# Kernel optimization log

Hardware: AMD Instinct MI355X
Metric: run time of the kernel (lower is better)

## Reference

```python
import jax, jax.numpy as jnp
import numpy as np

B, S, D = 8, 2048, 256
H, HD = 4, 64  # num_heads, head_size; H*HD == D


def setup_inputs() -> dict:
    key = jax.random.key(0)
    ks = jax.random.split(key, 9)
    scale = 0.02
    return {
        "x": jax.random.normal(ks[0], (B, S, D), dtype=jnp.float32),
        "Wq": jax.random.normal(ks[1], (D, H * HD), dtype=jnp.float32) * scale,
        "bq": jnp.zeros((H * HD,), dtype=jnp.float32),
        "Wk": jax.random.normal(ks[2], (D, H * HD), dtype=jnp.float32) * scale,
        "bk": jnp.zeros((H * HD,), dtype=jnp.float32),
        "Wv": jax.random.normal(ks[3], (D, H * HD), dtype=jnp.float32) * scale,
        "bv": jnp.zeros((H * HD,), dtype=jnp.float32),
        "Wo": jax.random.normal(ks[4], (H * HD, D), dtype=jnp.float32) * scale,
        "bo": jnp.zeros((D,), dtype=jnp.float32),
    }


def _split_heads(t):
    # [B, S, H*HD] -> [B, H, S, HD]
    b, s, _ = t.shape
    return t.reshape(b, s, H, HD).transpose(0, 2, 1, 3)


def reference(x, Wq, bq, Wk, bk, Wv, bv, Wo, bo):
    q = _split_heads(x @ Wq + bq)
    k = _split_heads(x @ Wk + bk)
    v = _split_heads(x @ Wv + bv)
    scores = jnp.einsum("bhqd,bhkd->bhqk", q, k) / jnp.sqrt(jnp.float32(HD))
    weights = jax.nn.softmax(scores, axis=-1)
    attn = jnp.einsum("bhqk,bhkd->bhqd", weights, v)  # [B, H, S, HD]
    concat = attn.transpose(0, 2, 1, 3).reshape(x.shape[0], -1, H * HD)
    return concat @ Wo + bo
```

## Files before the change

kernel.cpp:

```cpp
#include <hip/hip_runtime.h>
#include <hip/hip_bf16.h>

namespace {

constexpr int B_ = 8, S = 2048, D = 256, H = 4, HD = 64;
constexpr int M = B_ * S;

typedef __attribute__((ext_vector_type(8))) short bf16x8;
typedef __attribute__((ext_vector_type(4))) short bf16x4;
typedef __attribute__((ext_vector_type(2))) short bf16x2;
typedef __attribute__((ext_vector_type(4))) float f32x4;
typedef __attribute__((ext_vector_type(16))) float f32x16;
typedef __attribute__((ext_vector_type(4))) unsigned uint4v;

__device__ inline short f2bf(float x) {
  __hip_bfloat16 h = __float2bfloat16(x);
  short s;
  __builtin_memcpy(&s, &h, 2);
  return s;
}

__device__ inline f32x4 mfma16(bf16x8 a, bf16x8 b, f32x4 c) {
  return __builtin_amdgcn_mfma_f32_16x16x32_bf16(a, b, c, 0, 0, 0);
}
__device__ inline f32x16 mfma32(bf16x8 a, bf16x8 b, f32x16 c) {
  return __builtin_amdgcn_mfma_f32_32x32x16_bf16(a, b, c, 0, 0, 0);
}

__device__ inline float exp2a(float x) {
  float r;
  asm("v_exp_f32 %0, %1" : "=v"(r) : "v"(x));
  return r;
}

__device__ inline unsigned pkbf(float lo, float hi) {
  bf16x2 t;
  t[0] = f2bf(lo);
  t[1] = f2bf(hi);
  unsigned u;
  __builtin_memcpy(&u, &t, 4);
  return u;
}

__global__ __launch_bounds__(256) void prep_kernel(
    const float* __restrict__ x,
    const float* __restrict__ Wq, const float* __restrict__ Wk,
    const float* __restrict__ Wv, const float* __restrict__ Wo,
    short* __restrict__ xbf,
    short* __restrict__ WqT, short* __restrict__ WkT,
    short* __restrict__ WvT, short* __restrict__ WoT) {
  const int blk = blockIdx.x, t = threadIdx.x;
  if (blk < 64) {
    const int wq = blk >> 4, n0 = (blk & 15) * 16;
    const float* W = wq == 0 ? Wq : wq == 1 ? Wk : wq == 2 ? Wv : Wo;
    short* Wt = wq == 0 ? WqT : wq == 1 ? WkT : wq == 2 ? WvT : WoT;
#pragma unroll
    for (int j4 = 0; j4 < 4; ++j4) {
      float4 v = *(const float4*)(W + (size_t)t * 256 + n0 + j4 * 4);
      Wt[(n0 + j4 * 4 + 0) * 256 + t] = f2bf(v.x);
      Wt[(n0 + j4 * 4 + 1) * 256 + t] = f2bf(v.y);
      Wt[(n0 + j4 * 4 + 2) * 256 + t] = f2bf(v.z);
      Wt[(n0 + j4 * 4 + 3) * 256 + t] = f2bf(v.w);
    }
  } else {
    size_t base = ((size_t)(blk - 64) * 256 + t) * 8;
    float4 a = *(const float4*)(x + base);
    float4 b = *(const float4*)(x + base + 4);
    bf16x8 r;
    r[0] = f2bf(a.x); r[1] = f2bf(a.y); r[2] = f2bf(a.z); r[3] = f2bf(a.w);
    r[4] = f2bf(b.x); r[5] = f2bf(b.y); r[6] = f2bf(b.z); r[7] = f2bf(b.w);
    *(bf16x8*)(xbf + base) = r;
  }
}

__global__ __launch_bounds__(256) void gemm_qkv_kernel(
    const short* __restrict__ xbf,
    const short* __restrict__ WqT, const short* __restrict__ WkT,
    const short* __restrict__ WvT,
    const float* __restrict__ bq, const float* __restrict__ bk,
    const float* __restrict__ bv,
    short* __restrict__ Qo, short* __restrict__ Ko, short* __restrict__ Vt) {
  const int bx = blockIdx.x;
  const int which = blockIdx.y;
  const short* Wt = which == 0 ? WqT : which == 1 ? WkT : WvT;
  const float* bias = which == 0 ? bq : which == 1 ? bk : bv;

  __shared__ short Xs[2][64 * 32];
  __shared__ short Ws[2][256 * 32];

  const int tid = threadIdx.x;
  const int wid = tid >> 6, lane = tid & 63;
  const int l15 = lane & 15, l4 = lane >> 4;
  const int nt0 = wid * 4;

  const short* xsrc = xbf + ((size_t)(bx * 64 + (tid >> 2))) * 256 + (tid & 3) * 8;
  const short* wsrc = Wt + ((size_t)(tid >> 2)) * 256 + (tid & 3) * 8;
  short* xdst0 = &Xs[0][tid * 8];
  short* xdst1 = &Xs[1][tid * 8];
  short* wdst0 = &Ws[0][tid * 8];
  short* wdst1 = &Ws[1][tid * 8];

  bf16x8 xr, wr[4];
  xr = *(const bf16x8*)xsrc;
#pragma unroll
  for (int p = 0; p < 4; ++p) wr[p] = *(const bf16x8*)(wsrc + (size_t)p * 64 * 256);
  *(bf16x8*)xdst0 = xr;
#pragma unroll
  for (int p = 0; p < 4; ++p) *(bf16x8*)(wdst0 + p * 2048) = wr[p];
  __syncthreads();

  f32x4 acc[4][4];
#pragma unroll
  for (int i = 0; i < 4; ++i)
#pragma unroll
    for (int mh = 0; mh < 4; ++mh) acc[i][mh] = f32x4{0.f, 0.f, 0.f, 0.f};

  for (int ks = 0; ks < 8; ++ks) {
    const int cur = ks & 1;
    if (ks < 7) {
      xr = *(const bf16x8*)(xsrc + (ks + 1) * 32);
#pragma unroll
      for (int p = 0; p < 4; ++p)
        wr[p] = *(const bf16x8*)(wsrc + (size_t)p * 64 * 256 + (ks + 1) * 32);
    }
    bf16x8 wf[4], xf[4];
#pragma unroll
    for (int i = 0; i < 4; ++i)
      wf[i] = *(const bf16x8*)&Ws[cur][((nt0 + i) * 16 + l15) * 32 + l4 * 8];
#pragma unroll
    for (int mh = 0; mh < 4; ++mh)
      xf[mh] = *(const bf16x8*)&Xs[cur][(mh * 16 + l15) * 32 + l4 * 8];
    if (which == 2) {
#pragma unroll
      for (int i = 0; i < 4; ++i)
#pragma unroll
        for (int mh = 0; mh < 4; ++mh)
          acc[i][mh] = mfma16(xf[mh], wf[i], acc[i][mh]);
    } else {
#pragma unroll
      for (int i = 0; i < 4; ++i)
#pragma unroll
        for (int mh = 0; mh < 4; ++mh)
          acc[i][mh] = mfma16(wf[i], xf[mh], acc[i][mh]);
    }
    if (ks < 7) {
      short* xd = (cur ? xdst0 : xdst1);
      short* wd = (cur ? wdst0 : wdst1);
      *(bf16x8*)xd = xr;
#pragma unroll
      for (int p = 0; p < 4; ++p) *(bf16x8*)(wd + p * 2048) = wr[p];
    }
    __syncthreads();
  }

  if (which == 2) {
    const int m0 = bx * 64 + l4 * 4;
#pragma unroll
    for (int i = 0; i < 4; ++i) {
      const int n = (nt0 + i) * 16 + l15;
      const float bi = bias[n];
      const int h = n >> 6, d = n & 63;
#pragma unroll
      for (int mh = 0; mh < 4; ++mh) {
        const int m = m0 + mh * 16;
        const int bb = m >> 11, s0 = m & 2047;
        bf16x4 r;
        r[0] = f2bf(acc[i][mh][0] + bi);
        r[1] = f2bf(acc[i][mh][1] + bi);
        r[2] = f2bf(acc[i][mh][2] + bi);
        r[3] = f2bf(acc[i][mh][3] + bi);
        *(bf16x4*)(Vt + (((size_t)bb * H + h) * HD + d) * S + s0) = r;
      }
    }
  } else {
    const float scale = which == 0 ? 0.18033688011112042f : 1.0f;
    short* outp = which == 0 ? Qo : Ko;
#pragma unroll
    for (int i = 0; i < 4; ++i) {
      const int n0 = (nt0 + i) * 16 + l4 * 4;
      float4 bi = *(const float4*)(bias + n0);
      const int h = n0 >> 6, d0 = n0 & 63;
#pragma unroll
      for (int mh = 0; mh < 4; ++mh) {
        const int m = bx * 64 + mh * 16 + l15;
        const int bb = m >> 11, s = m & 2047;
        bf16x4 r;
        r[0] = f2bf((acc[i][mh][0] + bi.x) * scale);
        r[1] = f2bf((acc[i][mh][1] + bi.y) * scale);
        r[2] = f2bf((acc[i][mh][2] + bi.z) * scale);
        r[3] = f2bf((acc[i][mh][3] + bi.w) * scale);
        *(bf16x4*)(outp + (((size_t)bb * H + h) * S + s) * HD + d0) = r;
      }
    }
  }
}

__global__ __launch_bounds__(256) void gemm_out_kernel(
    const short* __restrict__ Abf, const short* __restrict__ WoT,
    const float* __restrict__ bo, float* __restrict__ out) {
  const int bx = blockIdx.x;
  __shared__ short Xs[2][64 * 32];
  __shared__ short Ws[2][256 * 32];

  const int tid = threadIdx.x;
  const int wid = tid >> 6, lane = tid & 63;
  const int l15 = lane & 15, l4 = lane >> 4;
  const int nt0 = wid * 4;

  const short* xsrc = Abf + ((size_t)(bx * 64 + (tid >> 2))) * 256 + (tid & 3) * 8;
  const short* wsrc = WoT + ((size_t)(tid >> 2)) * 256 + (tid & 3) * 8;
  short* xdst0 = &Xs[0][tid * 8];
  short* xdst1 = &Xs[1][tid * 8];
  short* wdst0 = &Ws[0][tid * 8];
  short* wdst1 = &Ws[1][tid * 8];

  bf16x8 xr, wr[4];
  xr = *(const bf16x8*)xsrc;
#pragma unroll
  for (int p = 0; p < 4; ++p) wr[p] = *(const bf16x8*)(wsrc + (size_t)p * 64 * 256);
  *(bf16x8*)xdst0 = xr;
#pragma unroll
  for (int p = 0; p < 4; ++p) *(bf16x8*)(wdst0 + p * 2048) = wr[p];
  __syncthreads();

  f32x4 acc[4][4];
#pragma unroll
  for (int i = 0; i < 4; ++i)
#pragma unroll
    for (int mh = 0; mh < 4; ++mh) acc[i][mh] = f32x4{0.f, 0.f, 0.f, 0.f};

  for (int ks = 0; ks < 8; ++ks) {
    const int cur = ks & 1;
    if (ks < 7) {
      xr = *(const bf16x8*)(xsrc + (ks + 1) * 32);
#pragma unroll
      for (int p = 0; p < 4; ++p)
        wr[p] = *(const bf16x8*)(wsrc + (size_t)p * 64 * 256 + (ks + 1) * 32);
    }
    bf16x8 wf[4], xf[4];
#pragma unroll
    for (int i = 0; i < 4; ++i)
      wf[i] = *(const bf16x8*)&Ws[cur][((nt0 + i) * 16 + l15) * 32 + l4 * 8];
#pragma unroll
    for (int mh = 0; mh < 4; ++mh)
      xf[mh] = *(const bf16x8*)&Xs[cur][(mh * 16 + l15) * 32 + l4 * 8];
#pragma unroll
    for (int i = 0; i < 4; ++i)
#pragma unroll
      for (int mh = 0; mh < 4; ++mh)
        acc[i][mh] = mfma16(wf[i], xf[mh], acc[i][mh]);
    if (ks < 7) {
      short* xd = (cur ? xdst0 : xdst1);
      short* wd = (cur ? wdst0 : wdst1);
      *(bf16x8*)xd = xr;
#pragma unroll
      for (int p = 0; p < 4; ++p) *(bf16x8*)(wd + p * 2048) = wr[p];
    }
    __syncthreads();
  }

#pragma unroll
  for (int i = 0; i < 4; ++i) {
    const int n0 = (nt0 + i) * 16 + l4 * 4;
    float4 bi = *(const float4*)(bo + n0);
#pragma unroll
    for (int mh = 0; mh < 4; ++mh) {
      const int m = bx * 64 + mh * 16 + l15;
      float4 r;
      r.x = acc[i][mh][0] + bi.x;
      r.y = acc[i][mh][1] + bi.y;
      r.z = acc[i][mh][2] + bi.z;
      r.w = acc[i][mh][3] + bi.w;
      *(float4*)(out + (size_t)m * 256 + n0) = r;
    }
  }
}

__global__ __launch_bounds__(256) void attn_kernel5(
    const short* __restrict__ Q, const short* __restrict__ K,
    const short* __restrict__ VT, short* __restrict__ Abf) {
  const int lin = blockIdx.x;
  const int bh = lin & 31;
  const int qt = lin >> 5;
  const int tid = threadIdx.x, wid = tid >> 6, lane = tid & 63;
  const int q31 = lane & 31, h = lane >> 5;

  __shared__ short Ks[2][64 * 128];
  __shared__ short Vs[2][64 * 128];

  const short* Kg = K + (size_t)bh * S * HD;
  const short* Vg = VT + (size_t)bh * HD * S;
  const int qrow = qt * 128 + wid * 32;

  const short* Qg = Q + ((size_t)bh * S + qrow + q31) * HD + h * 8;
  bf16x8 qf[4];
#pragma unroll
  for (int ds = 0; ds < 4; ++ds) qf[ds] = *(const bf16x8*)(Qg + ds * 16);

  const int srow = tid >> 2;
  const int scol = (tid & 3) * 16;
  const int swz = (srow & 15) * 8;
  const int c0 = scol ^ swz;
  const int c1 = (scol + 8) ^ swz;

  const int fs = (lane & 15) * 8;
  int kcol[4];
#pragma unroll
  for (int ds = 0; ds < 4; ++ds) kcol[ds] = (ds * 16 + h * 8) ^ fs;

  bf16x8 kr0, kr1, vr0, vr1;
  kr0 = *(const bf16x8*)(Kg + (size_t)srow * HD + scol);
  kr1 = *(const bf16x8*)(Kg + (size_t)srow * HD + scol + 8);
  vr0 = *(const bf16x8*)(Vg + (size_t)srow * S + scol);
  vr1 = *(const bf16x8*)(Vg + (size_t)srow * S + scol + 8);
  *(bf16x8*)&Ks[0][srow * 128 + c0] = kr0;
  *(bf16x8*)&Ks[0][srow * 128 + c1] = kr1;
  *(bf16x8*)&Vs[0][srow * 128 + c0] = vr0;
  *(bf16x8*)&Vs[0][srow * 128 + c1] = vr1;
  __syncthreads();

  f32x16 o0, o1;
#pragma unroll
  for (int i = 0; i < 16; ++i) { o0[i] = 0.f; o1[i] = 0.f; }
  float lacc = 0.f;

  for (int kt = 0; kt < S / 64; ++kt) {
    const int cur = kt & 1;
    if (kt + 1 < S / 64) {
      const short* Kn = Kg + (size_t)(kt + 1) * 64 * HD;
      const short* Vn = Vg + (size_t)(kt + 1) * 64;
      kr0 = *(const bf16x8*)(Kn + (size_t)srow * HD + scol);
      kr1 = *(const bf16x8*)(Kn + (size_t)srow * HD + scol + 8);
      vr0 = *(const bf16x8*)(Vn + (size_t)srow * S + scol);
      vr1 = *(const bf16x8*)(Vn + (size_t)srow * S + scol + 8);
    }

    f32x16 sc0, sc1;
#pragma unroll
    for (int i = 0; i < 16; ++i) { sc0[i] = 0.f; sc1[i] = 0.f; }
    __builtin_amdgcn_s_setprio(1);
#pragma unroll
    for (int ds = 0; ds < 4; ++ds) {
      bf16x8 k0 = *(const bf16x8*)&Ks[cur][(q31)*128 + kcol[ds]];
      bf16x8 k1 = *(const bf16x8*)&Ks[cur][(32 + q31) * 128 + kcol[ds]];
      sc0 = mfma32(k0, qf[ds], sc0);
      sc1 = mfma32(k1, qf[ds], sc1);
    }
    __builtin_amdgcn_s_setprio(0);

    bf16x8 pB[4];
#pragma unroll
    for (int win = 0; win < 2; ++win) {
      const f32x16& sc = win ? sc1 : sc0;
      float p[16];
      float a0 = 0.f, a1 = 0.f, a2 = 0.f, a3 = 0.f;
#pragma unroll
      for (int r = 0; r < 16; r += 4) {
        p[r + 0] = exp2a(sc[r + 0]);
        p[r + 1] = exp2a(sc[r + 1]);
        p[r + 2] = exp2a(sc[r + 2]);
        p[r + 3] = exp2a(sc[r + 3]);
        a0 += p[r + 0]; a1 += p[r + 1]; a2 += p[r + 2]; a3 += p[r + 3];
      }
      lacc += (a0 + a1) + (a2 + a3);
      unsigned w[8];
#pragma unroll
      for (int i = 0; i < 8; ++i) w[i] = pkbf(p[2 * i], p[2 * i + 1]);
      unsigned x0 = w[0], y0 = w[2];
      unsigned x1 = w[1], y1 = w[3];
      unsigned x2 = w[4], y2 = w[6];
      unsigned x3 = w[5], y3 = w[7];
      asm("v_permlane32_swap_b32 %0, %1" : "+v"(x0), "+v"(y0));
      asm("v_permlane32_swap_b32 %0, %1" : "+v"(x1), "+v"(y1));
      asm("v_permlane32_swap_b32 %0, %1" : "+v"(x2), "+v"(y2));
      asm("v_permlane32_swap_b32 %0, %1" : "+v"(x3), "+v"(y3));
      uint4v u0 = {x0, x1, y0, y1};
      uint4v u1 = {x2, x3, y2, y3};
      __builtin_memcpy(&pB[win * 2 + 0], &u0, 16);
      __builtin_memcpy(&pB[win * 2 + 1], &u1, 16);
    }

    __builtin_amdgcn_s_setprio(1);
#pragma unroll
    for (int kq = 0; kq < 4; ++kq) {
      const int vcol = (kq * 16 + h * 8) ^ fs;
      bf16x8 v0 = *(const bf16x8*)&Vs[cur][(q31)*128 + vcol];
      bf16x8 v1 = *(const bf16x8*)&Vs[cur][(32 + q31) * 128 + vcol];
      o0 = mfma32(v0, pB[kq], o0);
      o1 = mfma32(v1, pB[kq], o1);
    }
    __builtin_amdgcn_s_setprio(0);

    if (kt + 1 < S / 64) {
      const int nxt = cur ^ 1;
      *(bf16x8*)&Ks[nxt][srow * 128 + c0] = kr0;
      *(bf16x8*)&Ks[nxt][srow * 128 + c1] = kr1;
      *(bf16x8*)&Vs[nxt][srow * 128 + c0] = vr0;
      *(bf16x8*)&Vs[nxt][srow * 128 + c1] = vr1;
    }
    __syncthreads();
  }

  const float lall = lacc + __shfl_xor(lacc, 32);
  const float inv = 1.0f / lall;
  const int b = bh >> 2, hh = bh & 3;
  short* ap = Abf + ((size_t)b * S + qrow + q31) * 256 + hh * 64;
#pragma unroll
  for (int dt = 0; dt < 2; ++dt) {
    const f32x16& o = dt ? o1 : o0;
#pragma unroll
    for (int g = 0; g < 4; ++g) {
      const int d0 = dt * 32 + 8 * g + 4 * h;
      bf16x4 r;
      r[0] = f2bf(o[4 * g + 0] * inv);
      r[1] = f2bf(o[4 * g + 1] * inv);
      r[2] = f2bf(o[4 * g + 2] * inv);
      r[3] = f2bf(o[4 * g + 3] * inv);
      *(bf16x4*)(ap + d0) = r;
    }
  }
}

}

extern "C" void kernel_launch(void* const* d_in, const int* in_sizes, int n_in,
                              void* d_out, int out_size, void* d_ws, size_t ws_size,
                              hipStream_t stream) {
  const float* x  = (const float*)d_in[0];
  const float* Wq = (const float*)d_in[1];
  const float* bq = (const float*)d_in[2];
  const float* Wk = (const float*)d_in[3];
  const float* bk = (const float*)d_in[4];
  const float* Wv = (const float*)d_in[5];
  const float* bv = (const float*)d_in[6];
  const float* Wo = (const float*)d_in[7];
  const float* bo = (const float*)d_in[8];
  float* out = (float*)d_out;

  const size_t per = (size_t)M * D;
  short* xbf = (short*)d_ws;
  short* WqT = xbf + per;
  short* WkT = WqT + 256 * 256;
  short* WvT = WkT + 256 * 256;
  short* WoT = WvT + 256 * 256;
  short* Qbf = WoT + 256 * 256;
  short* Kbf = Qbf + per;
  short* Vt  = Kbf + per;
  short* Abf = Vt + per;

  prep_kernel<<<2112, 256, 0, stream>>>(x, Wq, Wk, Wv, Wo, xbf, WqT, WkT, WvT, WoT);
  gemm_qkv_kernel<<<dim3(256, 3), 256, 0, stream>>>(xbf, WqT, WkT, WvT, bq, bk, bv,
                                                    Qbf, Kbf, Vt);
  attn_kernel5<<<512, 256, 0, stream>>>(Qbf, Kbf, Vt, Abf);
  gemm_out_kernel<<<256, 256, 0, stream>>>(Abf, WoT, bo, out);
}
```

Baseline: 93.16 us.

## Fuse x bf16 conversion into QKV GEMM and use packed bf16 converts

Removes the separate fp32-to-bf16 conversion pass over x and instead loads fp32 x directly in the QKV GEMM, converting on the fly. This drops one kernel's worth of global write and read traffic for x. The prep kernel now only transposes and converts the weights. All bf16 conversions switch to the hardware v_cvt_pk_bf16_f32 instruction, and the attention kernel reuses precomputed kcol offsets for V reads. The trade-off is that the QKV GEMM reads twice as many bytes for x and repeats the conversion for each of the three projections.

```diff
diff --git a/kernel.cpp b/kernel.cpp
--- a/kernel.cpp
+++ b/kernel.cpp
@@ -8,7 +8,6 @@
 
 typedef __attribute__((ext_vector_type(8))) short bf16x8;
 typedef __attribute__((ext_vector_type(4))) short bf16x4;
-typedef __attribute__((ext_vector_type(2))) short bf16x2;
 typedef __attribute__((ext_vector_type(4))) float f32x4;
 typedef __attribute__((ext_vector_type(16))) float f32x16;
 typedef __attribute__((ext_vector_type(4))) unsigned uint4v;
@@ -33,48 +32,50 @@
   return r;
 }
 
-__device__ inline unsigned pkbf(float lo, float hi) {
-  bf16x2 t;
-  t[0] = f2bf(lo);
-  t[1] = f2bf(hi);
-  unsigned u;
-  __builtin_memcpy(&u, &t, 4);
-  return u;
-}
-
-__global__ __launch_bounds__(256) void prep_kernel(
-    const float* __restrict__ x,
+__device__ inline unsigned cvtpk(float lo, float hi) {
+  unsigned r;
+  asm("v_cvt_pk_bf16_f32 %0, %1, %2" : "=v"(r) : "v"(lo), "v"(hi));
+  return r;
+}
+
+__device__ inline bf16x4 pk4(float a, float b, float c, float d) {
+  unsigned lo = cvtpk(a, b), hi = cvtpk(c, d);
+  uint2 u{lo, hi};
+  bf16x4 r;
+  __builtin_memcpy(&r, &u, 8);
+  return r;
+}
+
+__device__ inline bf16x8 ld_cvt8(const float* p) {
+  float4 a = *(const float4*)p;
+  float4 b = *(const float4*)(p + 4);
+  uint4v u = {cvtpk(a.x, a.y), cvtpk(a.z, a.w), cvtpk(b.x, b.y), cvtpk(b.z, b.w)};
+  bf16x8 r;
+  __builtin_memcpy(&r, &u, 16);
+  return r;
+}
+
+__global__ __launch_bounds__(256) void prep_w_kernel(
     const float* __restrict__ Wq, const float* __restrict__ Wk,
     const float* __restrict__ Wv, const float* __restrict__ Wo,
-    short* __restrict__ xbf,
     short* __restrict__ WqT, short* __restrict__ WkT,
     short* __restrict__ WvT, short* __restrict__ WoT) {
   const int blk = blockIdx.x, t = threadIdx.x;
-  if (blk < 64) {
-    const int wq = blk >> 4, n0 = (blk & 15) * 16;
-    const float* W = wq == 0 ? Wq : wq == 1 ? Wk : wq == 2 ? Wv : Wo;
-    short* Wt = wq == 0 ? WqT : wq == 1 ? WkT : wq == 2 ? WvT : WoT;
-#pragma unroll
-    for (int j4 = 0; j4 < 4; ++j4) {
-      float4 v = *(const float4*)(W + (size_t)t * 256 + n0 + j4 * 4);
-      Wt[(n0 + j4 * 4 + 0) * 256 + t] = f2bf(v.x);
-      Wt[(n0 + j4 * 4 + 1) * 256 + t] = f2bf(v.y);
-      Wt[(n0 + j4 * 4 + 2) * 256 + t] = f2bf(v.z);
-      Wt[(n0 + j4 * 4 + 3) * 256 + t] = f2bf(v.w);
-    }
-  } else {
-    size_t base = ((size_t)(blk - 64) * 256 + t) * 8;
-    float4 a = *(const float4*)(x + base);
-    float4 b = *(const float4*)(x + base + 4);
-    bf16x8 r;
-    r[0] = f2bf(a.x); r[1] = f2bf(a.y); r[2] = f2bf(a.z); r[3] = f2bf(a.w);
-    r[4] = f2bf(b.x); r[5] = f2bf(b.y); r[6] = f2bf(b.z); r[7] = f2bf(b.w);
-    *(bf16x8*)(xbf + base) = r;
+  const int wq = blk >> 4, n0 = (blk & 15) * 16;
+  const float* W = wq == 0 ? Wq : wq == 1 ? Wk : wq == 2 ? Wv : Wo;
+  short* Wt = wq == 0 ? WqT : wq == 1 ? WkT : wq == 2 ? WvT : WoT;
+#pragma unroll
+  for (int j4 = 0; j4 < 4; ++j4) {
+    float4 v = *(const float4*)(W + (size_t)t * 256 + n0 + j4 * 4);
+    Wt[(n0 + j4 * 4 + 0) * 256 + t] = f2bf(v.x);
+    Wt[(n0 + j4 * 4 + 1) * 256 + t] = f2bf(v.y);
+    Wt[(n0 + j4 * 4 + 2) * 256 + t] = f2bf(v.z);
+    Wt[(n0 + j4 * 4 + 3) * 256 + t] = f2bf(v.w);
   }
 }
 
 __global__ __launch_bounds__(256) void gemm_qkv_kernel(
-    const short* __restrict__ xbf,
+    const float* __restrict__ x,
     const short* __restrict__ WqT, const short* __restrict__ WkT,
     const short* __restrict__ WvT,
     const float* __restrict__ bq, const float* __restrict__ bk,
@@ -93,7 +94,7 @@
   const int l15 = lane & 15, l4 = lane >> 4;
   const int nt0 = wid * 4;
 
-  const short* xsrc = xbf + ((size_t)(bx * 64 + (tid >> 2))) * 256 + (tid & 3) * 8;
+  const float* xsrc = x + ((size_t)(bx * 64 + (tid >> 2))) * 256 + (tid & 3) * 8;
   const short* wsrc = Wt + ((size_t)(tid >> 2)) * 256 + (tid & 3) * 8;
   short* xdst0 = &Xs[0][tid * 8];
   short* xdst1 = &Xs[1][tid * 8];
@@ -101,7 +102,7 @@
   short* wdst1 = &Ws[1][tid * 8];
 
   bf16x8 xr, wr[4];
-  xr = *(const bf16x8*)xsrc;
+  xr = ld_cvt8(xsrc);
 #pragma unroll
   for (int p = 0; p < 4; ++p) wr[p] = *(const bf16x8*)(wsrc + (size_t)p * 64 * 256);
   *(bf16x8*)xdst0 = xr;
@@ -118,7 +119,7 @@
   for (int ks = 0; ks < 8; ++ks) {
     const int cur = ks & 1;
     if (ks < 7) {
-      xr = *(const bf16x8*)(xsrc + (ks + 1) * 32);
+      xr = ld_cvt8(xsrc + (ks + 1) * 32);
 #pragma unroll
       for (int p = 0; p < 4; ++p)
         wr[p] = *(const bf16x8*)(wsrc + (size_t)p * 64 * 256 + (ks + 1) * 32);
@@ -164,11 +165,8 @@
       for (int mh = 0; mh < 4; ++mh) {
         const int m = m0 + mh * 16;
         const int bb = m >> 11, s0 = m & 2047;
-        bf16x4 r;
-        r[0] = f2bf(acc[i][mh][0] + bi);
-        r[1] = f2bf(acc[i][mh][1] + bi);
-        r[2] = f2bf(acc[i][mh][2] + bi);
-        r[3] = f2bf(acc[i][mh][3] + bi);
+        bf16x4 r = pk4(acc[i][mh][0] + bi, acc[i][mh][1] + bi,
+                       acc[i][mh][2] + bi, acc[i][mh][3] + bi);
         *(bf16x4*)(Vt + (((size_t)bb * H + h) * HD + d) * S + s0) = r;
       }
     }
@@ -184,11 +182,8 @@
       for (int mh = 0; mh < 4; ++mh) {
         const int m = bx * 64 + mh * 16 + l15;
         const int bb = m >> 11, s = m & 2047;
-        bf16x4 r;
-        r[0] = f2bf((acc[i][mh][0] + bi.x) * scale);
-        r[1] = f2bf((acc[i][mh][1] + bi.y) * scale);
-        r[2] = f2bf((acc[i][mh][2] + bi.z) * scale);
-        r[3] = f2bf((acc[i][mh][3] + bi.w) * scale);
+        bf16x4 r = pk4((acc[i][mh][0] + bi.x) * scale, (acc[i][mh][1] + bi.y) * scale,
+                       (acc[i][mh][2] + bi.z) * scale, (acc[i][mh][3] + bi.w) * scale);
         *(bf16x4*)(outp + (((size_t)bb * H + h) * S + s) * HD + d0) = r;
       }
     }
@@ -276,7 +271,7 @@
   }
 }
 
-__global__ __launch_bounds__(256) void attn_kernel5(
+__global__ __launch_bounds__(256) void attn_kernel6(
     const short* __restrict__ Q, const short* __restrict__ K,
     const short* __restrict__ VT, short* __restrict__ Abf) {
   const int lin = blockIdx.x;
@@ -365,7 +360,7 @@
       lacc += (a0 + a1) + (a2 + a3);
       unsigned w[8];
 #pragma unroll
-      for (int i = 0; i < 8; ++i) w[i] = pkbf(p[2 * i], p[2 * i + 1]);
+      for (int i = 0; i < 8; ++i) w[i] = cvtpk(p[2 * i], p[2 * i + 1]);
       unsigned x0 = w[0], y0 = w[2];
       unsigned x1 = w[1], y1 = w[3];
       unsigned x2 = w[4], y2 = w[6];
@@ -383,9 +378,8 @@
     __builtin_amdgcn_s_setprio(1);
 #pragma unroll
     for (int kq = 0; kq < 4; ++kq) {
-      const int vcol = (kq * 16 + h * 8) ^ fs;
-      bf16x8 v0 = *(const bf16x8*)&Vs[cur][(q31)*128 + vcol];
-      bf16x8 v1 = *(const bf16x8*)&Vs[cur][(32 + q31) * 128 + vcol];
+      bf16x8 v0 = *(const bf16x8*)&Vs[cur][(q31)*128 + kcol[kq]];
+      bf16x8 v1 = *(const bf16x8*)&Vs[cur][(32 + q31) * 128 + kcol[kq]];
       o0 = mfma32(v0, pB[kq], o0);
       o1 = mfma32(v1, pB[kq], o1);
     }
@@ -411,11 +405,8 @@
 #pragma unroll
     for (int g = 0; g < 4; ++g) {
       const int d0 = dt * 32 + 8 * g + 4 * h;
-      bf16x4 r;
-      r[0] = f2bf(o[4 * g + 0] * inv);
-      r[1] = f2bf(o[4 * g + 1] * inv);
-      r[2] = f2bf(o[4 * g + 2] * inv);
-      r[3] = f2bf(o[4 * g + 3] * inv);
+      bf16x4 r = pk4(o[4 * g + 0] * inv, o[4 * g + 1] * inv,
+                     o[4 * g + 2] * inv, o[4 * g + 3] * inv);
       *(bf16x4*)(ap + d0) = r;
     }
   }
@@ -438,8 +429,7 @@
   float* out = (float*)d_out;
 
   const size_t per = (size_t)M * D;
-  short* xbf = (short*)d_ws;
-  short* WqT = xbf + per;
+  short* WqT = (short*)d_ws;
   short* WkT = WqT + 256 * 256;
   short* WvT = WkT + 256 * 256;
   short* WoT = WvT + 256 * 256;
@@ -448,9 +438,9 @@
   short* Vt  = Kbf + per;
   short* Abf = Vt + per;
 
-  prep_kernel<<<2112, 256, 0, stream>>>(x, Wq, Wk, Wv, Wo, xbf, WqT, WkT, WvT, WoT);
-  gemm_qkv_kernel<<<dim3(256, 3), 256, 0, stream>>>(xbf, WqT, WkT, WvT, bq, bk, bv,
+  prep_w_kernel<<<64, 256, 0, stream>>>(Wq, Wk, Wv, Wo, WqT, WkT, WvT, WoT);
+  gemm_qkv_kernel<<<dim3(256, 3), 256, 0, stream>>>(x, WqT, WkT, WvT, bq, bk, bv,
                                                     Qbf, Kbf, Vt);
-  attn_kernel5<<<512, 256, 0, stream>>>(Qbf, Kbf, Vt, Abf);
+  attn_kernel6<<<512, 256, 0, stream>>>(Qbf, Kbf, Vt, Abf);
   gemm_out_kernel<<<256, 256, 0, stream>>>(Abf, WoT, bo, out);
 }
```

Measured after the change: 89.24 us. -4.2%, faster.
